# Kernel tuning notes

Hardware: AMD Instinct MI355X
Metric: run time of the kernel (lower is better)

Reference implementation:

```python
import jax, jax.numpy as jnp
import numpy as np

D_MODEL = 256
D_FF = 2048
H_HEADS = 8
N_LEVELS = 5
N_POINTS = 4
SPATIAL = [(128, 128), (64, 64), (32, 32), (16, 16), (8, 8)]
LV = sum(h * w for h, w in SPATIAL)  # 21824
LQ = 900
B = 8
D_HEAD = D_MODEL // H_HEADS


def _layer_norm(x, g, b, eps=1e-5):
    m = jnp.mean(x, -1, keepdims=True)
    v = jnp.mean((x - m) ** 2, -1, keepdims=True)
    return (x - m) * jax.lax.rsqrt(v + eps) * g + b


def _ms_deform_core(value, loc, attn_w):
    # value [B,Lv,H,D]; loc [B,Lq,H,L,P,2] normalized in [0,1]; attn_w [B,Lq,H,L,P]
    Bn, Lq = loc.shape[0], loc.shape[1]
    Dh = value.shape[-1]
    out = jnp.zeros((Bn, H_HEADS, Lq, Dh), value.dtype)
    start = 0
    for l, (Hh, Ww) in enumerate(SPATIAL):
        v = value[:, start:start + Hh * Ww].transpose(0, 2, 1, 3)  # [B,H,HW,D]
        start += Hh * Ww
        xy = loc[:, :, :, l]  # [B,Lq,H,P,2]
        # grid_sample align_corners=False: pixel = norm*size - 0.5
        x = xy[..., 0] * Ww - 0.5
        y = xy[..., 1] * Hh - 0.5
        x0 = jnp.floor(x); y0 = jnp.floor(y)
        fx = x - x0; fy = y - y0
        samp = jnp.zeros((Bn, H_HEADS, Lq * N_POINTS, Dh), value.dtype)
        corners = ((0, 0, (1 - fx) * (1 - fy)), (1, 0, fx * (1 - fy)),
                   (0, 1, (1 - fx) * fy), (1, 1, fx * fy))
        for dx, dy, wgt in corners:
            xc = x0 + dx; yc = y0 + dy
            valid = (xc >= 0) & (xc < Ww) & (yc >= 0) & (yc < Hh)  # zero padding
            idx = (jnp.clip(yc, 0, Hh - 1) * Ww + jnp.clip(xc, 0, Ww - 1)).astype(jnp.int32)
            wv = jnp.where(valid, wgt, 0.0)
            idx_r = idx.transpose(0, 2, 1, 3).reshape(Bn, H_HEADS, Lq * N_POINTS)
            wv_r = wv.transpose(0, 2, 1, 3).reshape(Bn, H_HEADS, Lq * N_POINTS)
            g = jnp.take_along_axis(v, idx_r[..., None], axis=2)  # [B,H,LqP,D]
            samp = samp + wv_r[..., None] * g
        samp = samp.reshape(Bn, H_HEADS, Lq, N_POINTS, Dh)
        aw = attn_w[:, :, :, l].transpose(0, 2, 1, 3)  # [B,H,Lq,P]
        out = out + (samp * aw[..., None]).sum(axis=3)
    return out.transpose(0, 2, 1, 3).reshape(Bn, Lq, H_HEADS * Dh)


def _forward(tgt, tgt_query_pos, tgt_reference_points, memory,
             sa_w_q, sa_b_q, sa_w_k, sa_b_k, sa_w_v, sa_b_v, sa_w_o, sa_b_o,
             ca_w_off, ca_b_off, ca_w_attn, ca_b_attn, ca_w_val, ca_b_val, ca_w_out, ca_b_out,
             ffn_w1, ffn_b1, ffn_w2, ffn_b2,
             ln1_g, ln1_b, ln2_g, ln2_b, ln3_g, ln3_b):
    Lq, Bn, C = tgt.shape
    scale = float(1.0 / np.sqrt(D_HEAD))
    # ---- self-attention (torch nn.MultiheadAttention, seq-first) ----
    qk = tgt + tgt_query_pos
    def heads(x):
        return x.reshape(Lq, Bn, H_HEADS, D_HEAD).transpose(1, 2, 0, 3)
    q = heads(qk @ sa_w_q + sa_b_q) * scale
    k = heads(qk @ sa_w_k + sa_b_k)
    v = heads(tgt @ sa_w_v + sa_b_v)
    attn = jax.nn.softmax(jnp.einsum('bhqd,bhkd->bhqk', q, k), axis=-1)
    o = jnp.einsum('bhqk,bhkd->bhqd', attn, v).transpose(2, 0, 1, 3).reshape(Lq, Bn, C)
    tgt = _layer_norm(tgt + (o @ sa_w_o + sa_b_o), ln2_g, ln2_b)
    # ---- multi-scale deformable cross-attention ----
    qb = (tgt + tgt_query_pos).transpose(1, 0, 2)            # [B,Lq,C]
    ref = tgt_reference_points.transpose(1, 0, 2, 3)         # [B,Lq,L,2]
    value = (memory.transpose(1, 0, 2) @ ca_w_val + ca_b_val).reshape(Bn, LV, H_HEADS, D_HEAD)
    off = (qb @ ca_w_off + ca_b_off).reshape(Bn, Lq, H_HEADS, N_LEVELS, N_POINTS, 2)
    aw = jax.nn.softmax((qb @ ca_w_attn + ca_b_attn).reshape(Bn, Lq, H_HEADS, N_LEVELS * N_POINTS), axis=-1)
    aw = aw.reshape(Bn, Lq, H_HEADS, N_LEVELS, N_POINTS)
    offset_normalizer = jnp.asarray([[w, h] for h, w in SPATIAL], tgt.dtype)  # (W,H) per level
    loc = ref[:, :, None, :, None, :] + off / offset_normalizer[None, None, None, :, None, :]
    samp = _ms_deform_core(value, loc, aw)                   # [B,Lq,C]
    o = (samp @ ca_w_out + ca_b_out).transpose(1, 0, 2)
    tgt = _layer_norm(tgt + o, ln1_g, ln1_b)
    # ---- FFN ----
    h = jax.nn.relu(tgt @ ffn_w1 + ffn_b1)
    tgt = _layer_norm(tgt + (h @ ffn_w2 + ffn_b2), ln3_g, ln3_b)
    return tgt


def setup_inputs() -> dict:
    key = jax.random.key(0)
    ks = iter(jax.random.split(key, 64))
    f32 = jnp.float32
    def nrm(shape, s=1.0):
        return (s * jax.random.normal(next(ks), shape)).astype(f32)
    inp = {}
    inp['tgt'] = nrm((LQ, B, D_MODEL))
    inp['tgt_query_pos'] = nrm((LQ, B, D_MODEL))
    inp['tgt_reference_points'] = jax.random.uniform(next(ks), (LQ, B, N_LEVELS, 2), f32)
    inp['memory'] = nrm((LV, B, D_MODEL))
    inp['memory_spatial_shapes'] = jnp.asarray(SPATIAL, jnp.int32)
    inp['memory_level_start_index'] = jnp.asarray(np.cumsum([0] + [h * w for h, w in SPATIAL[:-1]]), jnp.int32)
    for n, shp in [('sa_w_q', (D_MODEL, D_MODEL)), ('sa_w_k', (D_MODEL, D_MODEL)),
                   ('sa_w_v', (D_MODEL, D_MODEL)), ('sa_w_o', (D_MODEL, D_MODEL)),
                   ('ca_w_off', (D_MODEL, H_HEADS * N_LEVELS * N_POINTS * 2)),
                   ('ca_w_attn', (D_MODEL, H_HEADS * N_LEVELS * N_POINTS)),
                   ('ca_w_val', (D_MODEL, D_MODEL)), ('ca_w_out', (D_MODEL, D_MODEL)),
                   ('ffn_w1', (D_MODEL, D_FF)), ('ffn_w2', (D_FF, D_MODEL))]:
        inp[n] = nrm(shp, 0.02)
    for n, d in [('sa_b_q', D_MODEL), ('sa_b_k', D_MODEL), ('sa_b_v', D_MODEL), ('sa_b_o', D_MODEL),
                 ('ca_b_off', H_HEADS * N_LEVELS * N_POINTS * 2), ('ca_b_attn', H_HEADS * N_LEVELS * N_POINTS),
                 ('ca_b_val', D_MODEL), ('ca_b_out', D_MODEL), ('ffn_b1', D_FF), ('ffn_b2', D_MODEL)]:
        inp[n] = jnp.zeros((d,), f32)
    for n in ['ln1', 'ln2', 'ln3']:
        inp[n + '_g'] = jnp.ones((D_MODEL,), f32)
        inp[n + '_b'] = jnp.zeros((D_MODEL,), f32)
    return inp


def reference(tgt, tgt_query_pos, tgt_reference_points, memory,
              memory_spatial_shapes, memory_level_start_index,
              sa_w_q, sa_b_q, sa_w_k, sa_b_k, sa_w_v, sa_b_v, sa_w_o, sa_b_o,
              ca_w_off, ca_b_off, ca_w_attn, ca_b_attn, ca_w_val, ca_b_val, ca_w_out, ca_b_out,
              ffn_w1, ffn_b1, ffn_w2, ffn_b2,
              ln1_g, ln1_b, ln2_g, ln2_b, ln3_g, ln3_b):
    # spatial shapes / level start index are static metadata (SPATIAL), kept for API parity
    return _forward(tgt, tgt_query_pos, tgt_reference_points, memory,
                    sa_w_q, sa_b_q, sa_w_k, sa_b_k, sa_w_v, sa_b_v, sa_w_o, sa_b_o,
                    ca_w_off, ca_b_off, ca_w_attn, ca_b_attn, ca_w_val, ca_b_val, ca_w_out, ca_b_out,
                    ffn_w1, ffn_b1, ffn_w2, ffn_b2,
                    ln1_g, ln1_b, ln2_g, ln2_b, ln3_g, ln3_b)
```

## Files before the change

kernel.cpp:

```cpp
#include <hip/hip_runtime.h>
#include <hip/hip_bf16.h>
#include <type_traits>

#define LQ    900
#define BSZ   8
#define ROWS  (LQ*BSZ)
#define CDIM  256
#define QKS   512
#define OAS   480
#define NH    8
#define DH    32
#define LVTOT 21824
#define VROWS (LVTOT*BSZ)
#define DFF   2048

typedef unsigned short u16;
typedef short short8 __attribute__((ext_vector_type(8)));
typedef float f32x4 __attribute__((ext_vector_type(4)));

__device__ __forceinline__ u16 f2bf(float f) {
    __hip_bfloat16 h = __float2bfloat16(f);
    return *reinterpret_cast<u16*>(&h);
}
#define ATTN_SCALE 0.1767766952966369f
#define SWZ(r) (((r) & 3) ^ (((r) >> 2) & 3))

struct PrepArgs {
    const float* Wq; const float* Wk; const float* Wv; const float* Wo;
    const float* Wval; const float* Wout; const float* Woff; const float* Watt;
    const float* W1; const float* W2;
    u16* WqkT; u16* WvT; u16* WoT; u16* WvalT; u16* WoutT; u16* WoaT; u16* W1T; u16* W2T;
    const float* bq; const float* bk; const float* boff; const float* batt;
    float* bqk; float* boa;
};
__global__ __launch_bounds__(256) void prep_kernel(PrepArgs a) {
    __shared__ float t[32][33];
    const int id = blockIdx.x;
    if (id == 1528) {
        const int tx = threadIdx.x;
        if (tx < 256) { a.bqk[tx] = a.bq[tx] * ATTN_SCALE; a.bqk[256 + tx] = a.bk[tx]; }
        for (int i = tx; i < 320; i += 256) a.boa[i] = a.boff[i];
        if (tx < 160) a.boa[320 + tx] = a.batt[tx];
        return;
    }
    const float* W; u16* Wt; int K = 256, N = 256, nx = 8; float scale = 1.f; int r;
    if      (id < 64)   { W = a.Wq;   Wt = a.WqkT;           scale = ATTN_SCALE; r = id; }
    else if (id < 128)  { W = a.Wk;   Wt = a.WqkT + 256*256; r = id - 64; }
    else if (id < 192)  { W = a.Wv;   Wt = a.WvT;            r = id - 128; }
    else if (id < 256)  { W = a.Wo;   Wt = a.WoT;            r = id - 192; }
    else if (id < 320)  { W = a.Wval; Wt = a.WvalT;          r = id - 256; }
    else if (id < 384)  { W = a.Wout; Wt = a.WoutT;          r = id - 320; }
    else if (id < 464)  { W = a.Woff; Wt = a.WoaT;           N = 320; nx = 10; r = id - 384; }
    else if (id < 504)  { W = a.Watt; Wt = a.WoaT + 320*256; N = 160; nx = 5;  r = id - 464; }
    else if (id < 1016) { W = a.W1;   Wt = a.W1T;            N = 2048; nx = 64; r = id - 504; }
    else                { W = a.W2;   Wt = a.W2T;            K = 2048; N = 256; nx = 8; r = id - 1016; }
    const int n0 = (r % nx) * 32, k0 = (r / nx) * 32;
    const int tx = threadIdx.x & 31, ty = threadIdx.x >> 5;
    #pragma unroll
    for (int rr = ty; rr < 32; rr += 8)
        t[rr][tx] = W[(size_t)(k0 + rr) * N + n0 + tx];
    __syncthreads();
    #pragma unroll
    for (int rr = ty; rr < 32; rr += 8)
        Wt[(size_t)(n0 + rr) * K + k0 + tx] = f2bf(t[tx][rr] * scale);
}

__device__ __forceinline__ void stage512(const u16* __restrict__ src, u16* dst,
                                         int row0, int K, int k0, int maxrow, int tid) {
    const int sr = tid >> 2, sc = tid & 3;
    int grow = row0 + sr; if (grow > maxrow) grow = maxrow;
    const u16* gsrc = src + (size_t)grow * K + k0 + ((sc ^ SWZ(sr)) << 3);
    u16* ldst = dst + ((tid & ~63) << 3);
    __builtin_amdgcn_global_load_lds((const __attribute__((address_space(1))) void*)gsrc,
                                     (__attribute__((address_space(3))) void*)ldst, 16, 0, 0);
}

template<int ADD>
__device__ __forceinline__ void load_A8(float* f, const float* __restrict__ A,
                                        const float* __restrict__ A2,
                                        int arow, int K, int k0, int sc) {
    const float4* src = reinterpret_cast<const float4*>(&A[(size_t)arow * K + k0 + sc * 8]);
    float4 v0 = src[0], v1 = src[1];
    if (ADD) {
        const float4* s2 = reinterpret_cast<const float4*>(&A2[(size_t)arow * K + k0 + sc * 8]);
        float4 g0 = s2[0], g1 = s2[1];
        v0.x += g0.x; v0.y += g0.y; v0.z += g0.z; v0.w += g0.w;
        v1.x += g1.x; v1.y += g1.y; v1.z += g1.z; v1.w += g1.w;
    }
    f[0]=v0.x; f[1]=v0.y; f[2]=v0.z; f[3]=v0.w;
    f[4]=v1.x; f[5]=v1.y; f[6]=v1.z; f[7]=v1.w;
}

__device__ __forceinline__ void write_A8(u16* Adst, const float* f, int sr, int sc) {
    u16 t[8];
    #pragma unroll
    for (int i = 0; i < 8; ++i) t[i] = f2bf(f[i]);
    *reinterpret_cast<uint4*>(&Adst[sr*32 + ((sc ^ SWZ(sr)) * 8)]) =
        *reinterpret_cast<const uint4*>(t);
}

template<typename AT, int RELU, int ADD, typename OutT>
__device__ __forceinline__ void gemm_body(const AT* __restrict__ A, const float* __restrict__ A2,
                                          const u16* __restrict__ Wt, const float* __restrict__ bias,
                                          OutT* __restrict__ C, int M, int N, int K,
                                          int m0, int n0, int tid, u16* S) {
    const int lane = tid & 63;
    const int w = tid >> 6;
    const int wr = w >> 2, wc = w & 3;
    const int lr = lane & 15, lg = lane >> 4;
    const int sr = tid >> 2, sc = tid & 3;
    const int ns = K >> 5;
    const int arow = (m0 + sr < M) ? (m0 + sr) : (M - 1);

    f32x4 acc[4][2] = {};
    float fa[8];

    stage512(Wt, S + 8192, n0, K, 0, N - 1, tid);
    if constexpr (std::is_same<AT, float>::value) {
        load_A8<ADD>(fa, A, A2, arow, K, 0, sc);
        write_A8(S, fa, sr, sc);
    } else {
        stage512((const u16*)A, S, m0, K, 0, M - 1, tid);
    }
    __syncthreads();

    for (int t = 0; t < ns; ++t) {
        u16* Ac = S + ((t & 1) << 12);
        u16* Bc = S + 8192 + ((t & 1) << 12);
        const int nxt = (t + 1) & 1;
        if (t + 1 < ns) {
            stage512(Wt, S + 8192 + (nxt << 12), n0, K, (t + 1) << 5, N - 1, tid);
            if constexpr (std::is_same<AT, float>::value)
                load_A8<ADD>(fa, A, A2, arow, K, (t + 1) << 5, sc);
            else
                stage512((const u16*)A, S + (nxt << 12), m0, K, (t + 1) << 5, M - 1, tid);
        }
        short8 af[4], bf[2];
        #pragma unroll
        for (int i = 0; i < 4; ++i) {
            const int r = wr*64 + i*16 + lr;
            af[i] = *reinterpret_cast<const short8*>(&Ac[r*32 + ((lg ^ SWZ(r)) * 8)]);
        }
        #pragma unroll
        for (int j = 0; j < 2; ++j) {
            const int rb = wc*32 + j*16 + lr;
            bf[j] = *reinterpret_cast<const short8*>(&Bc[rb*32 + ((lg ^ SWZ(rb)) * 8)]);
        }
        #pragma unroll
        for (int i = 0; i < 4; ++i)
            #pragma unroll
            for (int j = 0; j < 2; ++j)
                acc[i][j] = __builtin_amdgcn_mfma_f32_16x16x32_bf16(af[i], bf[j], acc[i][j], 0, 0, 0);
        if (t + 1 < ns) {
            if constexpr (std::is_same<AT, float>::value)
                write_A8(S + (nxt << 12), fa, sr, sc);
        }
        __syncthreads();
    }

    if constexpr (std::is_same<OutT, float>::value) {
        #pragma unroll
        for (int j = 0; j < 2; ++j) {
            const int col = n0 + wc*32 + j*16 + lr;
            if (col >= N) continue;
            const float bcol = bias[col];
            #pragma unroll
            for (int i = 0; i < 4; ++i) {
                #pragma unroll
                for (int r = 0; r < 4; ++r) {
                    const int row = m0 + wr*64 + i*16 + lg*4 + r;
                    if (row >= M) continue;
                    float v = acc[i][j][r] + bcol;
                    if (RELU) v = fmaxf(v, 0.f);
                    C[(size_t)row * N + col] = v;
                }
            }
        }
    } else {
        __syncthreads();
        u16* Ct = S;
        #pragma unroll
        for (int j = 0; j < 2; ++j) {
            const int col = wc*32 + j*16 + lr;
            const float bcol = bias[n0 + col];
            #pragma unroll
            for (int i = 0; i < 4; ++i)
                #pragma unroll
                for (int r = 0; r < 4; ++r) {
                    float v = acc[i][j][r] + bcol;
                    if (RELU) v = fmaxf(v, 0.f);
                    Ct[(wr*64 + i*16 + lg*4 + r)*128 + col] = f2bf(v);
                }
        }
        __syncthreads();
        #pragma unroll
        for (int it = 0; it < 4; ++it) {
            const int idx = it*512 + tid;
            const int row = idx >> 4, cc = idx & 15;
            if (m0 + row < M)
                *reinterpret_cast<uint4*>(&C[(size_t)(m0 + row) * N + n0 + cc*8]) =
                    *reinterpret_cast<const uint4*>(&Ct[row*128 + cc*8]);
        }
    }
}

template<typename AT, int RELU, int ADD, typename OutT>
__global__ __launch_bounds__(512) void gemm_mfma(const AT* __restrict__ A, const float* __restrict__ A2,
                                                 const u16* __restrict__ Wt, const float* __restrict__ bias,
                                                 OutT* __restrict__ C, int M, int N, int K) {
    __shared__ __align__(16) u16 S[16384];
    gemm_body<AT, RELU, ADD, OutT>(A, A2, Wt, bias, C, M, N, K,
                                   blockIdx.y * 128, blockIdx.x * 128, threadIdx.x, S);
}

__global__ __launch_bounds__(512) void mgemm3_kernel(
        const float* __restrict__ Aval, const u16* __restrict__ WvalT, const float* __restrict__ bval, u16* __restrict__ Cval,
        const float* __restrict__ Aqk,  const float* __restrict__ Aqk2, const u16* __restrict__ WqkT,
        const float* __restrict__ bqk,  u16* __restrict__ Cqk,
        const float* __restrict__ Av,   const u16* __restrict__ WvT,   const float* __restrict__ bv, u16* __restrict__ Cv) {
    __shared__ __align__(16) u16 S[16384];
    int id = blockIdx.x;
    if (id < 2728) {
        gemm_body<float,0,0,u16>(Aval, nullptr, WvalT, bval, Cval, VROWS, 256, 256,
                                 (id >> 1) * 128, (id & 1) * 128, threadIdx.x, S);
    } else if (id < 2956) {
        id -= 2728;
        gemm_body<float,0,1,u16>(Aqk, Aqk2, WqkT, bqk, Cqk, ROWS, 512, 256,
                                 (id >> 2) * 128, (id & 3) * 128, threadIdx.x, S);
    } else {
        id -= 2956;
        gemm_body<float,0,0,u16>(Av, nullptr, WvT, bv, Cv, ROWS, 256, 256,
                                 (id >> 1) * 128, (id & 1) * 128, threadIdx.x, S);
    }
}

__global__ __launch_bounds__(256) void attn_mfma_kernel(const u16* __restrict__ qkb,
                                                        const u16* __restrict__ vb,
                                                        float* __restrict__ out) {
    __shared__ __align__(16) u16 Ks[64*32];
    __shared__ __align__(16) u16 Vt[32*64];
    const int bx = blockIdx.x;
    const int qt = bx & 7, h = (bx >> 3) & 7, b = bx >> 6;
    const int tid = threadIdx.x;
    const int w = tid >> 6, lane = tid & 63;
    const int lr = lane & 15, lg = lane >> 4;
    const int m0 = qt*128 + w*32;

    short8 qf[2];
    #pragma unroll
    for (int j = 0; j < 2; ++j) {
        int lq = m0 + j*16 + lr; if (lq > LQ-1) lq = LQ-1;
        qf[j] = *reinterpret_cast<const short8*>(&qkb[((size_t)lq*BSZ + b)*QKS + h*DH + lg*8]);
    }

    f32x4 o00 = {}, o01 = {}, o10 = {}, o11 = {};
    float m[2] = {-1e30f, -1e30f}, l[2] = {0.f, 0.f};
    const f32x4 zero = {};

    for (int kt = 0; kt < 15; ++kt) {
        __syncthreads();
        {
            const int key = tid >> 2, c = tid & 3;
            int kg = kt*64 + key; if (kg > LQ-1) kg = LQ-1;
            *reinterpret_cast<short8*>(&Ks[key*32 + ((c ^ ((key>>1)&3)) * 8)]) =
                *reinterpret_cast<const short8*>(&qkb[((size_t)kg*BSZ + b)*QKS + 256 + h*DH + c*8]);
            short8 vv = *reinterpret_cast<const short8*>(&vb[((size_t)kg*BSZ + b)*CDIM + h*DH + c*8]);
            const u16* pv = reinterpret_cast<const u16*>(&vv);
            #pragma unroll
            for (int e = 0; e < 8; ++e) {
                const int dh = c*8 + e;
                Vt[dh*64 + (((key>>3) ^ (dh&7)) * 8) + (key&7)] = pv[e];
            }
        }
        __syncthreads();

        f32x4 s[4][2];
        #pragma unroll
        for (int i = 0; i < 4; ++i) {
            const int key = i*16 + lr;
            short8 kf = *reinterpret_cast<const short8*>(&Ks[key*32 + ((lg ^ ((key>>1)&3)) * 8)]);
            s[i][0] = __builtin_amdgcn_mfma_f32_16x16x32_bf16(kf, qf[0], zero, 0, 0, 0);
            s[i][1] = __builtin_amdgcn_mfma_f32_16x16x32_bf16(kf, qf[1], zero, 0, 0, 0);
        }
        const int lim = LQ - kt*64 - lg*4;
        #pragma unroll
        for (int i = 0; i < 4; ++i)
            #pragma unroll
            for (int r = 0; r < 4; ++r)
                if (i*16 + r >= lim) { s[i][0][r] = -1e30f; s[i][1][r] = -1e30f; }

        #pragma unroll
        for (int j = 0; j < 2; ++j) {
            float mx = -1e30f;
            #pragma unroll
            for (int i = 0; i < 4; ++i)
                #pragma unroll
                for (int r = 0; r < 4; ++r) mx = fmaxf(mx, s[i][j][r]);
            mx = fmaxf(mx, __shfl_xor(mx, 16));
            mx = fmaxf(mx, __shfl_xor(mx, 32));
            const float mn = fmaxf(m[j], mx);
            const float corr = __expf(m[j] - mn);
            float sum = 0.f;
            #pragma unroll
            for (int i = 0; i < 4; ++i)
                #pragma unroll
                for (int r = 0; r < 4; ++r) {
                    float p = __expf(s[i][j][r] - mn);
                    s[i][j][r] = p;
                    sum += p;
                }
            sum += __shfl_xor(sum, 16);
            sum += __shfl_xor(sum, 32);
            l[j] = l[j]*corr + sum;
            m[j] = mn;
            if (j == 0) { o00 *= corr; o10 *= corr; }
            else        { o01 *= corr; o11 *= corr; }
        }

        short8 pb[2][2];
        #pragma unroll
        for (int kh = 0; kh < 2; ++kh)
            #pragma unroll
            for (int j = 0; j < 2; ++j) {
                u16 t[8];
                #pragma unroll
                for (int e = 0; e < 4; ++e) {
                    t[e]   = f2bf(s[2*kh][j][e]);
                    t[e+4] = f2bf(s[2*kh+1][j][e]);
                }
                pb[kh][j] = *reinterpret_cast<short8*>(t);
            }

        #pragma unroll
        for (int ip = 0; ip < 2; ++ip) {
            const int dh = ip*16 + lr;
            #pragma unroll
            for (int kh = 0; kh < 2; ++kh) {
                u16 t[8];
                const int c0 = (kh*4 + (lg>>1)) ^ (dh&7);
                const int c1 = (kh*4 + 2 + (lg>>1)) ^ (dh&7);
                *reinterpret_cast<uint2*>(&t[0]) =
                    *reinterpret_cast<const uint2*>(&Vt[dh*64 + c0*8 + (lg&1)*4]);
                *reinterpret_cast<uint2*>(&t[4]) =
                    *reinterpret_cast<const uint2*>(&Vt[dh*64 + c1*8 + (lg&1)*4]);
                short8 vf = *reinterpret_cast<short8*>(t);
                if (ip == 0) {
                    o00 = __builtin_amdgcn_mfma_f32_16x16x32_bf16(vf, pb[kh][0], o00, 0, 0, 0);
                    o01 = __builtin_amdgcn_mfma_f32_16x16x32_bf16(vf, pb[kh][1], o01, 0, 0, 0);
                } else {
                    o10 = __builtin_amdgcn_mfma_f32_16x16x32_bf16(vf, pb[kh][0], o10, 0, 0, 0);
                    o11 = __builtin_amdgcn_mfma_f32_16x16x32_bf16(vf, pb[kh][1], o11, 0, 0, 0);
                }
            }
        }
    }

    #pragma unroll
    for (int j = 0; j < 2; ++j) {
        const int lq = m0 + j*16 + lr;
        if (lq >= LQ) continue;
        const float inv = 1.f / l[j];
        float* op = &out[((size_t)lq*BSZ + b)*CDIM + h*DH];
        #pragma unroll
        for (int r = 0; r < 4; ++r) {
            const f32x4& a0 = (j == 0) ? o00 : o01;
            const f32x4& a1 = (j == 0) ? o10 : o11;
            op[lg*4 + r]      = a0[r] * inv;
            op[16 + lg*4 + r] = a1[r] * inv;
        }
    }
}

__global__ __launch_bounds__(256) void ln_res_kernel(const float* __restrict__ xin,
                                                     const float* __restrict__ res,
                                                     const float* __restrict__ g,
                                                     const float* __restrict__ beta,
                                                     float* __restrict__ out) {
    const int row  = blockIdx.x * 4 + (threadIdx.x >> 6);
    const int lane = threadIdx.x & 63;
    const size_t base = (size_t)row * CDIM + lane * 4;
    float4 a = *reinterpret_cast<const float4*>(&xin[base]);
    float4 r = *reinterpret_cast<const float4*>(&res[base]);
    float x0 = a.x+r.x, x1 = a.y+r.y, x2 = a.z+r.z, x3 = a.w+r.w;
    float s = x0+x1+x2+x3;
    #pragma unroll
    for (int o = 1; o < 64; o <<= 1) s += __shfl_xor(s, o);
    float mean = s * (1.f/256.f);
    float d0 = x0-mean, d1 = x1-mean, d2 = x2-mean, d3 = x3-mean;
    float sq = d0*d0 + d1*d1 + d2*d2 + d3*d3;
    #pragma unroll
    for (int o = 1; o < 64; o <<= 1) sq += __shfl_xor(sq, o);
    float rs = rsqrtf(sq * (1.f/256.f) + 1e-5f);
    float4 gg = *reinterpret_cast<const float4*>(&g[lane*4]);
    float4 bb = *reinterpret_cast<const float4*>(&beta[lane*4]);
    float4 o4 = make_float4(d0*rs*gg.x+bb.x, d1*rs*gg.y+bb.y, d2*rs*gg.z+bb.z, d3*rs*gg.w+bb.w);
    *reinterpret_cast<float4*>(&out[base]) = o4;
}

__global__ __launch_bounds__(256) void softmax20_kernel(float* __restrict__ oab) {
    int item = blockIdx.x * 256 + threadIdx.x;
    if (item >= ROWS * NH) return;
    int row = item >> 3, h = item & 7;
    float* p = &oab[(size_t)row*OAS + 320 + h*20];
    float mx = -1e30f;
    float e[20];
    #pragma unroll
    for (int j = 0; j < 20; ++j) mx = fmaxf(mx, p[j]);
    float sum = 0.f;
    #pragma unroll
    for (int j = 0; j < 20; ++j) { e[j] = __expf(p[j] - mx); sum += e[j]; }
    float inv = 1.f / sum;
    #pragma unroll
    for (int j = 0; j < 20; ++j) p[j] = e[j] * inv;
}

__global__ __launch_bounds__(256) void msdeform_kernel(const u16* __restrict__ value,
                                                       const float* __restrict__ oab,
                                                       const float* __restrict__ refp,
                                                       float* __restrict__ samp) {
    const int gid = blockIdx.x * 32 + (threadIdx.x >> 3);
    const int ch  = (threadIdx.x & 7) * 4;
    const int h   = gid & 7;
    const int row = gid >> 3;
    const int b   = row & 7;
    const int WL[5] = {128, 64, 32, 16, 8};
    const int SL[5] = {0, 16384, 20480, 21504, 21760};
    const u16* vbase = value + h*DH + ch;
    float a0 = 0.f, a1 = 0.f, a2 = 0.f, a3 = 0.f;
    #pragma unroll
    for (int l = 0; l < 5; ++l) {
        const float2 r2 = *reinterpret_cast<const float2*>(&refp[((size_t)row*5 + l)*2]);
        const int W = WL[l];
        const float Wf = (float)W;
        #pragma unroll
        for (int p = 0; p < 4; ++p) {
            const float2 o2 = *reinterpret_cast<const float2*>(&oab[(size_t)row*OAS + ((h*5 + l)*4 + p)*2]);
            const float aw = oab[(size_t)row*OAS + 320 + h*20 + l*4 + p];
            const float x = (r2.x + o2.x / Wf) * Wf - 0.5f;
            const float y = (r2.y + o2.y / Wf) * Wf - 0.5f;
            const float x0f = floorf(x), y0f = floorf(y);
            const float fx = x - x0f, fy = y - y0f;
            const int x0 = (int)x0f, y0 = (int)y0f;
            float wx0 = (1.f - fx) * aw, wx1 = fx * aw;
            float fy0 = 1.f - fy, fy1 = fy;
            if (x0 < 0 || x0 >= W)       wx0 = 0.f;
            if (x0+1 < 0 || x0+1 >= W)   wx1 = 0.f;
            if (y0 < 0 || y0 >= W)       fy0 = 0.f;
            if (y0+1 < 0 || y0+1 >= W)   fy1 = 0.f;
            const float w00 = wx0*fy0, w10 = wx1*fy0, w01 = wx0*fy1, w11 = wx1*fy1;
            const int xc0 = min(max(x0, 0), W-1),   xc1 = min(max(x0+1, 0), W-1);
            const int yc0 = min(max(y0, 0), W-1),   yc1 = min(max(y0+1, 0), W-1);
            const int r0 = SL[l] + yc0*W, r1 = SL[l] + yc1*W;
            const int o00i = ((r0 + xc0)*BSZ + b) * CDIM;
            const int o10i = ((r0 + xc1)*BSZ + b) * CDIM;
            const int o01i = ((r1 + xc0)*BSZ + b) * CDIM;
            const int o11i = ((r1 + xc1)*BSZ + b) * CDIM;
            const uint2 u00 = *reinterpret_cast<const uint2*>(vbase + o00i);
            const uint2 u10 = *reinterpret_cast<const uint2*>(vbase + o10i);
            const uint2 u01 = *reinterpret_cast<const uint2*>(vbase + o01i);
            const uint2 u11 = *reinterpret_cast<const uint2*>(vbase + o11i);
            a0 += w00 * __uint_as_float(u00.x << 16) + w10 * __uint_as_float(u10.x << 16)
                + w01 * __uint_as_float(u01.x << 16) + w11 * __uint_as_float(u11.x << 16);
            a1 += w00 * __uint_as_float(u00.x & 0xffff0000u) + w10 * __uint_as_float(u10.x & 0xffff0000u)
                + w01 * __uint_as_float(u01.x & 0xffff0000u) + w11 * __uint_as_float(u11.x & 0xffff0000u);
            a2 += w00 * __uint_as_float(u00.y << 16) + w10 * __uint_as_float(u10.y << 16)
                + w01 * __uint_as_float(u01.y << 16) + w11 * __uint_as_float(u11.y << 16);
            a3 += w00 * __uint_as_float(u00.y & 0xffff0000u) + w10 * __uint_as_float(u10.y & 0xffff0000u)
                + w01 * __uint_as_float(u01.y & 0xffff0000u) + w11 * __uint_as_float(u11.y & 0xffff0000u);
        }
    }
    float4 o4 = make_float4(a0, a1, a2, a3);
    *reinterpret_cast<float4*>(&samp[(size_t)row*CDIM + h*DH + ch]) = o4;
}

extern "C" void kernel_launch(void* const* d_in, const int* in_sizes, int n_in,
                              void* d_out, int out_size, void* d_ws, size_t ws_size,
                              hipStream_t stream) {
    (void)in_sizes; (void)n_in; (void)out_size; (void)ws_size;
    const float* tgt    = (const float*)d_in[0];
    const float* qpos   = (const float*)d_in[1];
    const float* refpts = (const float*)d_in[2];
    const float* memory = (const float*)d_in[3];
    const float* Wq  = (const float*)d_in[6];
    const float* Wk  = (const float*)d_in[7];
    const float* Wv  = (const float*)d_in[8];
    const float* Wo  = (const float*)d_in[9];
    const float* Woff= (const float*)d_in[10];
    const float* Watt= (const float*)d_in[11];
    const float* Wval= (const float*)d_in[12];
    const float* Wout= (const float*)d_in[13];
    const float* W1  = (const float*)d_in[14];
    const float* W2  = (const float*)d_in[15];
    const float* bq  = (const float*)d_in[16];
    const float* bk  = (const float*)d_in[17];
    const float* bv  = (const float*)d_in[18];
    const float* bo  = (const float*)d_in[19];
    const float* boff= (const float*)d_in[20];
    const float* batt= (const float*)d_in[21];
    const float* bval= (const float*)d_in[22];
    const float* bout= (const float*)d_in[23];
    const float* b1  = (const float*)d_in[24];
    const float* b2  = (const float*)d_in[25];
    const float* ln1g= (const float*)d_in[26];
    const float* ln1b= (const float*)d_in[27];
    const float* ln2g= (const float*)d_in[28];
    const float* ln2b= (const float*)d_in[29];
    const float* ln3g= (const float*)d_in[30];
    const float* ln3b= (const float*)d_in[31];
    float* out = (float*)d_out;

    char* ws = (char*)d_ws;
    const size_t RB = (size_t)ROWS * CDIM * 4;
    float* tgt2  = (float*)(ws + 0*RB);
    float* tgt3  = (float*)(ws + 1*RB);
    float* qk    = (float*)(ws + 2*RB);
    float* vbuf  = (float*)(ws + 3*RB);
    float* abuf  = (float*)(ws + 4*RB);
    u16* qkb = (u16*)(ws + 5*RB);
    u16* vb  = (u16*)(ws + 5*RB + (size_t)ROWS*QKS*2);
    float* oab = (float*)(ws + 5*RB + (size_t)ROWS*QKS*2 + (size_t)ROWS*CDIM*2);
    char* wsm = ws + 5*RB + (size_t)ROWS*QKS*2 + (size_t)ROWS*CDIM*2 + (size_t)ROWS*OAS*4;
    u16* WqkT  = (u16*)(wsm);
    u16* WvT   = (u16*)(wsm + 262144);
    u16* WoT   = (u16*)(wsm + 262144 + 1*131072);
    u16* WvalT = (u16*)(wsm + 262144 + 2*131072);
    u16* WoutT = (u16*)(wsm + 262144 + 3*131072);
    u16* WoaT  = (u16*)(wsm + 262144 + 4*131072);
    u16* W1T   = (u16*)(wsm + 2*262144 + 4*131072);
    u16* W2T   = (u16*)(wsm + 2*262144 + 4*131072 + 1048576);
    float* bqk = (float*)(wsm + 2*262144 + 4*131072 + 2097152);
    float* boa = (float*)(wsm + 2*262144 + 4*131072 + 2097152 + 2048);
    char* big  = wsm + 2*262144 + 4*131072 + 2097152 + 4096;
    u16* valb  = (u16*)big;
    u16* ffnh  = (u16*)(big + (size_t)VROWS*CDIM*2);

    const dim3 blk(256);
    const dim3 blk512(512);

    PrepArgs pa = { Wq, Wk, Wv, Wo, Wval, Wout, Woff, Watt, W1, W2,
                    WqkT, WvT, WoT, WvalT, WoutT, WoaT, W1T, W2T,
                    bq, bk, boff, batt, bqk, boa };
    prep_kernel<<<dim3(1529), blk, 0, stream>>>(pa);

    mgemm3_kernel<<<dim3(3070), blk512, 0, stream>>>(
        memory, WvalT, bval, valb,
        tgt, qpos, WqkT, bqk, qkb,
        tgt, WvT, bv, vb);

    attn_mfma_kernel<<<dim3(512), blk, 0, stream>>>(qkb, vb, abuf);
    gemm_mfma<float,0,0,float><<<dim3(2,57), blk512, 0, stream>>>(abuf, nullptr, WoT, bo, qk, ROWS, CDIM, CDIM);
    ln_res_kernel<<<dim3(ROWS/4), blk, 0, stream>>>(qk, tgt, ln2g, ln2b, tgt2);

    gemm_mfma<float,0,1,float><<<dim3(4,57), blk512, 0, stream>>>(tgt2, qpos, WoaT, boa, oab, ROWS, OAS, CDIM);
    softmax20_kernel<<<dim3((ROWS*NH+255)/256), blk, 0, stream>>>(oab);
    msdeform_kernel<<<dim3(ROWS*NH/32), blk, 0, stream>>>(valb, oab, refpts, vbuf);
    gemm_mfma<float,0,0,float><<<dim3(2,57), blk512, 0, stream>>>(vbuf, nullptr, WoutT, bout, qk, ROWS, CDIM, CDIM);
    ln_res_kernel<<<dim3(ROWS/4), blk, 0, stream>>>(qk, tgt2, ln1g, ln1b, tgt3);

    gemm_mfma<float,1,0,u16><<<dim3(16,57), blk512, 0, stream>>>(tgt3, nullptr, W1T, b1, ffnh, ROWS, DFF, CDIM);
    gemm_mfma<u16,0,0,float><<<dim3(2,57),  blk512, 0, stream>>>(ffnh, nullptr, W2T, b2, abuf, ROWS, CDIM, DFF);
    ln_res_kernel<<<dim3(ROWS/4), blk, 0, stream>>>(abuf, tgt3, ln3g, ln3b, out);
}
```

Measured before the change: 323.6 us.

## Deepen GEMM prefetch pipeline to four stages and unfuse query-position add

The shared GEMM body is rewritten as a 4-deep software pipeline. A and B tiles are loaded three k-steps ahead, and explicit vmcnt/lgkmcnt waits plus raw barriers replace the per-step __syncthreads double buffer. The fused A+A2 query-position add is removed from the GEMM and done instead by a separate vector-add kernel writing a new workspace buffer, which simplifies the A-load path. This aims to hide global-load latency in the MFMA GEMMs. In exchange it uses more LDS (48KB) and registers, adds two extra elementwise kernel passes, and relies on hand-tuned waitcnt counts that are fragile.

```diff
diff --git a/kernel.cpp b/kernel.cpp
--- a/kernel.cpp
+++ b/kernel.cpp
@@ -24,6 +24,17 @@
 }
 #define ATTN_SCALE 0.1767766952966369f
 #define SWZ(r) (((r) & 3) ^ (((r) >> 2) & 3))
+
+__global__ __launch_bounds__(256) void addvec_kernel(const float* __restrict__ a,
+                                                     const float* __restrict__ b,
+                                                     float* __restrict__ c, int n4) {
+    int i = blockIdx.x * 256 + threadIdx.x;
+    if (i < n4) {
+        float4 x = reinterpret_cast<const float4*>(a)[i];
+        float4 y = reinterpret_cast<const float4*>(b)[i];
+        reinterpret_cast<float4*>(c)[i] = make_float4(x.x+y.x, x.y+y.y, x.z+y.z, x.w+y.w);
+    }
+}
 
 struct PrepArgs {
     const float* Wq; const float* Wk; const float* Wv; const float* Wo;
@@ -65,44 +76,12 @@
         Wt[(size_t)(n0 + rr) * K + k0 + tx] = f2bf(t[tx][rr] * scale);
 }
 
-__device__ __forceinline__ void stage512(const u16* __restrict__ src, u16* dst,
-                                         int row0, int K, int k0, int maxrow, int tid) {
-    const int sr = tid >> 2, sc = tid & 3;
-    int grow = row0 + sr; if (grow > maxrow) grow = maxrow;
-    const u16* gsrc = src + (size_t)grow * K + k0 + ((sc ^ SWZ(sr)) << 3);
-    u16* ldst = dst + ((tid & ~63) << 3);
-    __builtin_amdgcn_global_load_lds((const __attribute__((address_space(1))) void*)gsrc,
-                                     (__attribute__((address_space(3))) void*)ldst, 16, 0, 0);
-}
-
-template<int ADD>
-__device__ __forceinline__ void load_A8(float* f, const float* __restrict__ A,
-                                        const float* __restrict__ A2,
-                                        int arow, int K, int k0, int sc) {
-    const float4* src = reinterpret_cast<const float4*>(&A[(size_t)arow * K + k0 + sc * 8]);
-    float4 v0 = src[0], v1 = src[1];
-    if (ADD) {
-        const float4* s2 = reinterpret_cast<const float4*>(&A2[(size_t)arow * K + k0 + sc * 8]);
-        float4 g0 = s2[0], g1 = s2[1];
-        v0.x += g0.x; v0.y += g0.y; v0.z += g0.z; v0.w += g0.w;
-        v1.x += g1.x; v1.y += g1.y; v1.z += g1.z; v1.w += g1.w;
-    }
-    f[0]=v0.x; f[1]=v0.y; f[2]=v0.z; f[3]=v0.w;
-    f[4]=v1.x; f[5]=v1.y; f[6]=v1.z; f[7]=v1.w;
-}
-
-__device__ __forceinline__ void write_A8(u16* Adst, const float* f, int sr, int sc) {
-    u16 t[8];
-    #pragma unroll
-    for (int i = 0; i < 8; ++i) t[i] = f2bf(f[i]);
-    *reinterpret_cast<uint4*>(&Adst[sr*32 + ((sc ^ SWZ(sr)) * 8)]) =
-        *reinterpret_cast<const uint4*>(t);
-}
-
-template<typename AT, int RELU, int ADD, typename OutT>
-__device__ __forceinline__ void gemm_body(const AT* __restrict__ A, const float* __restrict__ A2,
-                                          const u16* __restrict__ Wt, const float* __restrict__ bias,
-                                          OutT* __restrict__ C, int M, int N, int K,
+template<typename AT, int RELU, typename OutT>
+__device__ __forceinline__ void gemm_body(const AT* __restrict__ A,
+                                          const u16* __restrict__ Wt,
+                                          const float* __restrict__ bias,
+                                          OutT* __restrict__ C,
+                                          int M, int N, int K,
                                           int m0, int n0, int tid, u16* S) {
     const int lane = tid & 63;
     const int w = tid >> 6;
@@ -111,52 +90,80 @@
     const int sr = tid >> 2, sc = tid & 3;
     const int ns = K >> 5;
     const int arow = (m0 + sr < M) ? (m0 + sr) : (M - 1);
+    int brow = n0 + sr; if (brow > N - 1) brow = N - 1;
+    const u16* Bsrc = Wt + (size_t)brow * K + ((sc ^ SWZ(sr)) << 3);
+    u16* Bdst = S + 8192 + ((tid & ~63) << 3);
 
     f32x4 acc[4][2] = {};
-    float fa[8];
-
-    stage512(Wt, S + 8192, n0, K, 0, N - 1, tid);
-    if constexpr (std::is_same<AT, float>::value) {
-        load_A8<ADD>(fa, A, A2, arow, K, 0, sc);
-        write_A8(S, fa, sr, sc);
-    } else {
-        stage512((const u16*)A, S, m0, K, 0, M - 1, tid);
-    }
-    __syncthreads();
-
-    for (int t = 0; t < ns; ++t) {
-        u16* Ac = S + ((t & 1) << 12);
-        u16* Bc = S + 8192 + ((t & 1) << 12);
-        const int nxt = (t + 1) & 1;
-        if (t + 1 < ns) {
-            stage512(Wt, S + 8192 + (nxt << 12), n0, K, (t + 1) << 5, N - 1, tid);
-            if constexpr (std::is_same<AT, float>::value)
-                load_A8<ADD>(fa, A, A2, arow, K, (t + 1) << 5, sc);
-            else
-                stage512((const u16*)A, S + (nxt << 12), m0, K, (t + 1) << 5, M - 1, tid);
-        }
-        short8 af[4], bf[2];
-        #pragma unroll
-        for (int i = 0; i < 4; ++i) {
-            const int r = wr*64 + i*16 + lr;
-            af[i] = *reinterpret_cast<const short8*>(&Ac[r*32 + ((lg ^ SWZ(r)) * 8)]);
-        }
-        #pragma unroll
-        for (int j = 0; j < 2; ++j) {
-            const int rb = wc*32 + j*16 + lr;
-            bf[j] = *reinterpret_cast<const short8*>(&Bc[rb*32 + ((lg ^ SWZ(rb)) * 8)]);
-        }
-        #pragma unroll
-        for (int i = 0; i < 4; ++i)
-            #pragma unroll
-            for (int j = 0; j < 2; ++j)
-                acc[i][j] = __builtin_amdgcn_mfma_f32_16x16x32_bf16(af[i], bf[j], acc[i][j], 0, 0, 0);
-        if (t + 1 < ns) {
-            if constexpr (std::is_same<AT, float>::value)
-                write_A8(S + (nxt << 12), fa, sr, sc);
-        }
-        __syncthreads();
-    }
+    float4 fal[4], fah[4];
+    short8 fab[4];
+
+#define LOADA(I, KK) do { \
+    if constexpr (std::is_same<AT, float>::value) { \
+        const float4* s_ = reinterpret_cast<const float4*>((const float*)A + (size_t)arow*K + (KK)*32 + sc*8); \
+        fal[I] = s_[0]; fah[I] = s_[1]; \
+    } else { \
+        fab[I] = *reinterpret_cast<const short8*>((const u16*)A + (size_t)arow*K + (KK)*32 + sc*8); \
+    } } while (0)
+
+#define STAGEB(BUF, KK) \
+    __builtin_amdgcn_global_load_lds((const __attribute__((address_space(1))) void*)(Bsrc + (size_t)(KK)*32), \
+        (__attribute__((address_space(3))) void*)(Bdst + (BUF)*4096), 16, 0, 0)
+
+#define WRITEA(BUF, I) do { \
+    u16 t_[8]; \
+    if constexpr (std::is_same<AT, float>::value) { \
+        t_[0]=f2bf(fal[I].x); t_[1]=f2bf(fal[I].y); t_[2]=f2bf(fal[I].z); t_[3]=f2bf(fal[I].w); \
+        t_[4]=f2bf(fah[I].x); t_[5]=f2bf(fah[I].y); t_[6]=f2bf(fah[I].z); t_[7]=f2bf(fah[I].w); \
+    } else { *reinterpret_cast<short8*>(t_) = fab[I]; } \
+    *reinterpret_cast<uint4*>(&S[(BUF)*4096 + sr*32 + ((sc ^ SWZ(sr)) * 8)]) = *reinterpret_cast<const uint4*>(t_); \
+    } while (0)
+
+#define WAITVM() do { \
+    if constexpr (std::is_same<AT, float>::value) asm volatile("s_waitcnt vmcnt(7)" ::: "memory"); \
+    else asm volatile("s_waitcnt vmcnt(5)" ::: "memory"); } while (0)
+
+#define COMPUTE(CUR, BB) do { \
+    short8 af_[4], bf_[2]; \
+    _Pragma("unroll") for (int i = 0; i < 4; ++i) { \
+        const int r_ = wr*64 + i*16 + lr; \
+        af_[i] = *reinterpret_cast<const short8*>(&S[(CUR)*4096 + r_*32 + ((lg ^ SWZ(r_)) * 8)]); } \
+    _Pragma("unroll") for (int j = 0; j < 2; ++j) { \
+        const int rb_ = wc*32 + j*16 + lr; \
+        bf_[j] = *reinterpret_cast<const short8*>(&S[8192 + (BB)*4096 + rb_*32 + ((lg ^ SWZ(rb_)) * 8)]); } \
+    _Pragma("unroll") for (int i = 0; i < 4; ++i) \
+        _Pragma("unroll") for (int j = 0; j < 2; ++j) \
+            acc[i][j] = __builtin_amdgcn_mfma_f32_16x16x32_bf16(af_[i], bf_[j], acc[i][j], 0, 0, 0); \
+    } while (0)
+
+#define STEP(c) do { \
+    asm volatile("s_waitcnt lgkmcnt(0)" ::: "memory"); \
+    __builtin_amdgcn_s_barrier(); \
+    int kp_ = k4 + (c) + 3; if (kp_ > ns - 1) kp_ = ns - 1; \
+    LOADA(((c)+3)&3, kp_); STAGEB(((c)+3)&3, kp_); \
+    WAITVM(); \
+    WRITEA(((c)+1)&1, ((c)+1)&3); \
+    COMPUTE((c)&1, (c)&3); } while (0)
+
+    LOADA(0, 0); STAGEB(0, 0);
+    LOADA(1, 1); STAGEB(1, 1);
+    LOADA(2, 2); STAGEB(2, 2);
+    WAITVM();
+    WRITEA(0, 0);
+
+    for (int q = 0; q < (ns >> 2); ++q) {
+        const int k4 = q << 2;
+        STEP(0); STEP(1); STEP(2); STEP(3);
+    }
+    asm volatile("s_waitcnt vmcnt(0) lgkmcnt(0)" ::: "memory");
+    __builtin_amdgcn_s_barrier();
+
+#undef LOADA
+#undef STAGEB
+#undef WRITEA
+#undef WAITVM
+#undef COMPUTE
+#undef STEP
 
     if constexpr (std::is_same<OutT, float>::value) {
         #pragma unroll
@@ -177,7 +184,6 @@
             }
         }
     } else {
-        __syncthreads();
         u16* Ct = S;
         #pragma unroll
         for (int j = 0; j < 2; ++j) {
@@ -204,34 +210,27 @@
     }
 }
 
-template<typename AT, int RELU, int ADD, typename OutT>
-__global__ __launch_bounds__(512) void gemm_mfma(const AT* __restrict__ A, const float* __restrict__ A2,
-                                                 const u16* __restrict__ Wt, const float* __restrict__ bias,
+template<typename AT, int RELU, typename OutT>
+__global__ __launch_bounds__(512) void gemm_mfma(const AT* __restrict__ A,
+                                                 const u16* __restrict__ Wt,
+                                                 const float* __restrict__ bias,
                                                  OutT* __restrict__ C, int M, int N, int K) {
-    __shared__ __align__(16) u16 S[16384];
-    gemm_body<AT, RELU, ADD, OutT>(A, A2, Wt, bias, C, M, N, K,
-                                   blockIdx.y * 128, blockIdx.x * 128, threadIdx.x, S);
+    __shared__ __align__(16) u16 S[24576];
+    gemm_body<AT, RELU, OutT>(A, Wt, bias, C, M, N, K,
+                              blockIdx.y * 128, blockIdx.x * 128, threadIdx.x, S);
 }
 
 __global__ __launch_bounds__(512) void mgemm3_kernel(
-        const float* __restrict__ Aval, const u16* __restrict__ WvalT, const float* __restrict__ bval, u16* __restrict__ Cval,
-        const float* __restrict__ Aqk,  const float* __restrict__ Aqk2, const u16* __restrict__ WqkT,
-        const float* __restrict__ bqk,  u16* __restrict__ Cqk,
-        const float* __restrict__ Av,   const u16* __restrict__ WvT,   const float* __restrict__ bv, u16* __restrict__ Cv) {
-    __shared__ __align__(16) u16 S[16384];
+        const float* __restrict__ memory, const u16* __restrict__ WvalT, const float* __restrict__ bval, u16* __restrict__ Cval,
+        const float* __restrict__ qkin,   const u16* __restrict__ WqkT,  const float* __restrict__ bqk,  u16* __restrict__ Cqk,
+        const float* __restrict__ tgtv,   const u16* __restrict__ WvT,   const float* __restrict__ bv,   u16* __restrict__ Cv) {
+    __shared__ __align__(16) u16 S[24576];
     int id = blockIdx.x;
-    if (id < 2728) {
-        gemm_body<float,0,0,u16>(Aval, nullptr, WvalT, bval, Cval, VROWS, 256, 256,
-                                 (id >> 1) * 128, (id & 1) * 128, threadIdx.x, S);
-    } else if (id < 2956) {
-        id -= 2728;
-        gemm_body<float,0,1,u16>(Aqk, Aqk2, WqkT, bqk, Cqk, ROWS, 512, 256,
-                                 (id >> 2) * 128, (id & 3) * 128, threadIdx.x, S);
-    } else {
-        id -= 2956;
-        gemm_body<float,0,0,u16>(Av, nullptr, WvT, bv, Cv, ROWS, 256, 256,
-                                 (id >> 1) * 128, (id & 1) * 128, threadIdx.x, S);
-    }
+    const float* A; const u16* Wt; const float* bias; u16* C; int M, N, m0, n0;
+    if (id < 2728)      { A = memory; Wt = WvalT; bias = bval; C = Cval; M = VROWS; N = 256; m0 = (id >> 1)*128; n0 = (id & 1)*128; }
+    else if (id < 2956) { id -= 2728; A = qkin; Wt = WqkT; bias = bqk; C = Cqk; M = ROWS; N = 512; m0 = (id >> 2)*128; n0 = (id & 3)*128; }
+    else                { id -= 2956; A = tgtv; Wt = WvT; bias = bv; C = Cv; M = ROWS; N = 256; m0 = (id >> 1)*128; n0 = (id & 1)*128; }
+    gemm_body<float, 0, u16>(A, Wt, bias, C, M, N, 256, m0, n0, threadIdx.x, S);
 }
 
 __global__ __launch_bounds__(256) void attn_mfma_kernel(const u16* __restrict__ qkb,
@@ -516,10 +515,11 @@
     float* qk    = (float*)(ws + 2*RB);
     float* vbuf  = (float*)(ws + 3*RB);
     float* abuf  = (float*)(ws + 4*RB);
-    u16* qkb = (u16*)(ws + 5*RB);
-    u16* vb  = (u16*)(ws + 5*RB + (size_t)ROWS*QKS*2);
-    float* oab = (float*)(ws + 5*RB + (size_t)ROWS*QKS*2 + (size_t)ROWS*CDIM*2);
-    char* wsm = ws + 5*RB + (size_t)ROWS*QKS*2 + (size_t)ROWS*CDIM*2 + (size_t)ROWS*OAS*4;
+    float* qkin  = (float*)(ws + 5*RB);
+    u16* qkb = (u16*)(ws + 6*RB);
+    u16* vb  = (u16*)(ws + 6*RB + (size_t)ROWS*QKS*2);
+    float* oab = (float*)(ws + 6*RB + (size_t)ROWS*QKS*2 + (size_t)ROWS*CDIM*2);
+    char* wsm = ws + 6*RB + (size_t)ROWS*QKS*2 + (size_t)ROWS*CDIM*2 + (size_t)ROWS*OAS*4;
     u16* WqkT  = (u16*)(wsm);
     u16* WvT   = (u16*)(wsm + 262144);
     u16* WoT   = (u16*)(wsm + 262144 + 1*131072);
@@ -536,28 +536,31 @@
 
     const dim3 blk(256);
     const dim3 blk512(512);
+    const int n4 = ROWS * CDIM / 4;
 
     PrepArgs pa = { Wq, Wk, Wv, Wo, Wval, Wout, Woff, Watt, W1, W2,
                     WqkT, WvT, WoT, WvalT, WoutT, WoaT, W1T, W2T,
                     bq, bk, boff, batt, bqk, boa };
     prep_kernel<<<dim3(1529), blk, 0, stream>>>(pa);
 
+    addvec_kernel<<<dim3((n4+255)/256), blk, 0, stream>>>(tgt, qpos, qkin, n4);
     mgemm3_kernel<<<dim3(3070), blk512, 0, stream>>>(
         memory, WvalT, bval, valb,
-        tgt, qpos, WqkT, bqk, qkb,
+        qkin, WqkT, bqk, qkb,
         tgt, WvT, bv, vb);
 
     attn_mfma_kernel<<<dim3(512), blk, 0, stream>>>(qkb, vb, abuf);
-    gemm_mfma<float,0,0,float><<<dim3(2,57), blk512, 0, stream>>>(abuf, nullptr, WoT, bo, qk, ROWS, CDIM, CDIM);
+    gemm_mfma<float,0,float><<<dim3(2,57), blk512, 0, stream>>>(abuf, WoT, bo, qk, ROWS, CDIM, CDIM);
     ln_res_kernel<<<dim3(ROWS/4), blk, 0, stream>>>(qk, tgt, ln2g, ln2b, tgt2);
 
-    gemm_mfma<float,0,1,float><<<dim3(4,57), blk512, 0, stream>>>(tgt2, qpos, WoaT, boa, oab, ROWS, OAS, CDIM);
+    addvec_kernel<<<dim3((n4+255)/256), blk, 0, stream>>>(tgt2, qpos, qkin, n4);
+    gemm_mfma<float,0,float><<<dim3(4,57), blk512, 0, stream>>>(qkin, WoaT, boa, oab, ROWS, OAS, CDIM);
     softmax20_kernel<<<dim3((ROWS*NH+255)/256), blk, 0, stream>>>(oab);
     msdeform_kernel<<<dim3(ROWS*NH/32), blk, 0, stream>>>(valb, oab, refpts, vbuf);
-    gemm_mfma<float,0,0,float><<<dim3(2,57), blk512, 0, stream>>>(vbuf, nullptr, WoutT, bout, qk, ROWS, CDIM, CDIM);
+    gemm_mfma<float,0,float><<<dim3(2,57), blk512, 0, stream>>>(vbuf, WoutT, bout, qk, ROWS, CDIM, CDIM);
     ln_res_kernel<<<dim3(ROWS/4), blk, 0, stream>>>(qk, tgt2, ln1g, ln1b, tgt3);
 
-    gemm_mfma<float,1,0,u16><<<dim3(16,57), blk512, 0, stream>>>(tgt3, nullptr, W1T, b1, ffnh, ROWS, DFF, CDIM);
-    gemm_mfma<u16,0,0,float><<<dim3(2,57),  blk512, 0, stream>>>(ffnh, nullptr, W2T, b2, abuf, ROWS, CDIM, DFF);
+    gemm_mfma<float,1,u16><<<dim3(16,57), blk512, 0, stream>>>(tgt3, W1T, b1, ffnh, ROWS, DFF, CDIM);
+    gemm_mfma<u16,0,float><<<dim3(2,57),  blk512, 0, stream>>>(ffnh, W2T, b2, abuf, ROWS, CDIM, DFF);
     ln_res_kernel<<<dim3(ROWS/4), blk, 0, stream>>>(abuf, tgt3, ln3g, ln3b, out);
 }
```

Result: no change. 328.3 us (+1.5%).
